# Performance work log

Hardware: AMD Instinct MI355X
Metric: run time of the kernel (lower is better)

The kernel has to match this reference:

```python
import jax, jax.numpy as jnp
import numpy as np

EPS = 1e-12  # matches torch F.normalize default eps
WEIGHT = jnp.array([1.0, 1.0, 1.0], dtype=jnp.float32)  # per-channel loss weights


def _l2norm(x, axis):
    # torch F.normalize: x / max(||x||_2, eps)
    n = jnp.sqrt(jnp.sum(x * x, axis=axis, keepdims=True))
    return x / jnp.maximum(n, EPS)


def setup_inputs() -> dict:
    key = jax.random.key(0)
    k1, k2 = jax.random.split(key)
    shape = (16, 3, 512, 512)  # [B, C, H, W]
    return {
        "x": jax.random.normal(k1, shape, dtype=jnp.float32),
        "ref": jax.random.normal(k2, shape, dtype=jnp.float32),
    }


def reference(x, ref):
    # trace(rownorm(A) @ rownorm(B)^T) == sum(rownorm(A) * rownorm(B));
    # trace(colnorm(A)^T @ colnorm(B)) == sum(colnorm(A) * colnorm(B)).
    B, C, H, W = x.shape
    # per (batch, channel) traces, vectorized over all dims
    a = jnp.sum(_l2norm(x, -1) * _l2norm(ref, -1), axis=(-2, -1)) / H  # [B, C]
    b = jnp.sum(_l2norm(x, -2) * _l2norm(ref, -2), axis=(-2, -1)) / W  # [B, C]
    a = -jnp.sum(a * WEIGHT) / B
    b = -jnp.sum(b * WEIGHT) / B
    return a + b
```

## Files before the change

kernel.cpp:

```cpp
#include <hip/hip_runtime.h>

#define B_N 16
#define C_N 3
#define H_N 512
#define W_N 512
#define PLANES (B_N * C_N)
#define ROWS_PER_BLOCK 32
#define CHUNKS (H_N / ROWS_PER_BLOCK)
#define NBLK (PLANES * CHUNKS)
#define STATS3 (W_N * 3)
#define SCALE (-1.0f / 8192.0f)
#define EPS_F 1e-12f

__global__ __launch_bounds__(256) void spl_main_kernel(
    const float* __restrict__ x, const float* __restrict__ r,
    float* __restrict__ colpart, float* __restrict__ rowpart) {
    const int p     = blockIdx.x / CHUNKS;
    const int chunk = blockIdx.x % CHUNKS;
    const int wave  = threadIdx.x >> 6;
    const int lane  = threadIdx.x & 63;

    const float* xp = x + (size_t)p * (H_N * W_N);
    const float* rp = r + (size_t)p * (H_N * W_N);

    float cxx[8] = {0, 0, 0, 0, 0, 0, 0, 0};
    float crr[8] = {0, 0, 0, 0, 0, 0, 0, 0};
    float cxr[8] = {0, 0, 0, 0, 0, 0, 0, 0};
    float rowacc = 0.0f;

    const int r0 = chunk * ROWS_PER_BLOCK;
    for (int j = 0; j < ROWS_PER_BLOCK / 4; ++j) {
        const int row = r0 + wave + 4 * j;
        const float4* xr4 = (const float4*)(xp + (size_t)row * W_N);
        const float4* rr4 = (const float4*)(rp + (size_t)row * W_N);
        const float4 xa = xr4[lane];
        const float4 xb = xr4[lane + 64];
        const float4 ra = rr4[lane];
        const float4 rb = rr4[lane + 64];

        cxx[0] += xa.x * xa.x; cxx[1] += xa.y * xa.y; cxx[2] += xa.z * xa.z; cxx[3] += xa.w * xa.w;
        cxx[4] += xb.x * xb.x; cxx[5] += xb.y * xb.y; cxx[6] += xb.z * xb.z; cxx[7] += xb.w * xb.w;
        crr[0] += ra.x * ra.x; crr[1] += ra.y * ra.y; crr[2] += ra.z * ra.z; crr[3] += ra.w * ra.w;
        crr[4] += rb.x * rb.x; crr[5] += rb.y * rb.y; crr[6] += rb.z * rb.z; crr[7] += rb.w * rb.w;
        cxr[0] += xa.x * ra.x; cxr[1] += xa.y * ra.y; cxr[2] += xa.z * ra.z; cxr[3] += xa.w * ra.w;
        cxr[4] += xb.x * rb.x; cxr[5] += xb.y * rb.y; cxr[6] += xb.z * rb.z; cxr[7] += xb.w * rb.w;

        float sxx = cxx[0] + cxx[1] + cxx[2] + cxx[3] + cxx[4] + cxx[5] + cxx[6] + cxx[7];
        float srr = crr[0] + crr[1] + crr[2] + crr[3] + crr[4] + crr[5] + crr[6] + crr[7];
        float sxr = cxr[0] + cxr[1] + cxr[2] + cxr[3] + cxr[4] + cxr[5] + cxr[6] + cxr[7];
        sxx = xa.x * xa.x + xa.y * xa.y + xa.z * xa.z + xa.w * xa.w
            + xb.x * xb.x + xb.y * xb.y + xb.z * xb.z + xb.w * xb.w;
        srr = ra.x * ra.x + ra.y * ra.y + ra.z * ra.z + ra.w * ra.w
            + rb.x * rb.x + rb.y * rb.y + rb.z * rb.z + rb.w * rb.w;
        sxr = xa.x * ra.x + xa.y * ra.y + xa.z * ra.z + xa.w * ra.w
            + xb.x * rb.x + xb.y * rb.y + xb.z * rb.z + xb.w * rb.w;
        #pragma unroll
        for (int m = 32; m > 0; m >>= 1) {
            sxx += __shfl_down(sxx, m, 64);
            srr += __shfl_down(srr, m, 64);
            sxr += __shfl_down(sxr, m, 64);
        }
        if (lane == 0) {
            const float nx = fmaxf(sqrtf(sxx), EPS_F);
            const float nr = fmaxf(sqrtf(srr), EPS_F);
            rowacc += sxr / (nx * nr);
        }
    }

    __shared__ float smem[4][STATS3];
    #pragma unroll
    for (int k = 0; k < 4; ++k) {
        const int c0 = 4 * lane + k;
        const int c1 = c0 + 256;
        smem[wave][c0 * 3 + 0] = cxx[k];
        smem[wave][c0 * 3 + 1] = crr[k];
        smem[wave][c0 * 3 + 2] = cxr[k];
        smem[wave][c1 * 3 + 0] = cxx[4 + k];
        smem[wave][c1 * 3 + 1] = crr[4 + k];
        smem[wave][c1 * 3 + 2] = cxr[4 + k];
    }
    __shared__ float rowsums[4];
    if (lane == 0) rowsums[wave] = rowacc;
    __syncthreads();

    float* cp = colpart + (size_t)blockIdx.x * STATS3;
    #pragma unroll
    for (int k = 0; k < 6; ++k) {
        const int e = threadIdx.x + 256 * k;
        cp[e] = smem[0][e] + smem[1][e] + smem[2][e] + smem[3][e];
    }
    if (threadIdx.x == 0)
        rowpart[blockIdx.x] = rowsums[0] + rowsums[1] + rowsums[2] + rowsums[3];
}

__global__ __launch_bounds__(256) void spl_reduce_kernel(
    const float* __restrict__ colpart, const float* __restrict__ rowpart,
    float* __restrict__ planesum) {
    const int p = blockIdx.x;
    float acc[6] = {0, 0, 0, 0, 0, 0};
    const float* base = colpart + (size_t)p * CHUNKS * STATS3;
    for (int c = 0; c < CHUNKS; ++c) {
        const float* bc = base + c * STATS3;
        #pragma unroll
        for (int k = 0; k < 6; ++k) acc[k] += bc[threadIdx.x + 256 * k];
    }
    __shared__ float sums[STATS3];
    #pragma unroll
    for (int k = 0; k < 6; ++k) sums[threadIdx.x + 256 * k] = acc[k];
    __syncthreads();

    float term = 0.0f;
    #pragma unroll
    for (int k = 0; k < 2; ++k) {
        const int col = threadIdx.x + 256 * k;
        const float sxx = sums[col * 3 + 0];
        const float srr = sums[col * 3 + 1];
        const float sxr = sums[col * 3 + 2];
        term += sxr / (fmaxf(sqrtf(sxx), EPS_F) * fmaxf(sqrtf(srr), EPS_F));
    }
    if (threadIdx.x < CHUNKS) term += rowpart[p * CHUNKS + threadIdx.x];

    #pragma unroll
    for (int m = 32; m > 0; m >>= 1) term += __shfl_down(term, m, 64);
    __shared__ float ws[4];
    if ((threadIdx.x & 63) == 0) ws[threadIdx.x >> 6] = term;
    __syncthreads();
    if (threadIdx.x == 0) planesum[p] = ws[0] + ws[1] + ws[2] + ws[3];
}

__global__ void spl_final_kernel(const float* __restrict__ planesum,
                                 float* __restrict__ out) {
    float v = (threadIdx.x < PLANES) ? planesum[threadIdx.x] : 0.0f;
    #pragma unroll
    for (int m = 32; m > 0; m >>= 1) v += __shfl_down(v, m, 64);
    if (threadIdx.x == 0) out[0] = SCALE * v;
}

extern "C" void kernel_launch(void* const* d_in, const int* in_sizes, int n_in,
                              void* d_out, int out_size, void* d_ws, size_t ws_size,
                              hipStream_t stream) {
    const float* x   = (const float*)d_in[0];
    const float* ref = (const float*)d_in[1];
    float* out = (float*)d_out;

    float* colpart  = (float*)d_ws;
    float* rowpart  = colpart + (size_t)NBLK * STATS3;
    float* planesum = rowpart + NBLK;

    spl_main_kernel<<<NBLK, 256, 0, stream>>>(x, ref, colpart, rowpart);
    spl_reduce_kernel<<<PLANES, 256, 0, stream>>>(colpart, rowpart, planesum);
    spl_final_kernel<<<1, 64, 0, stream>>>(planesum, out);
}
```

Baseline: 120.9 us.

## Batch row reductions after loop and fuse final reduction via last-block counter

Row statistics are now stored per row, and the cross-lane shuffle reductions run once after the fully unrolled row loop, instead of serially inside each iteration. That lets the loads for all rows be issued together rather than waiting on shuffle chains. The separate final kernel is removed: the reduce kernel uses an atomic counter, reset by the main kernel, so the last block to finish sums the plane totals. This saves one kernel launch but adds atomics and raises register pressure from the unrolled loop.

Measured after the change: 137.8 us. +13.9%, slower.

```diff
diff --git a/kernel.cpp b/kernel.cpp
--- a/kernel.cpp
+++ b/kernel.cpp
@@ -14,7 +14,11 @@
 
 __global__ __launch_bounds__(256) void spl_main_kernel(
     const float* __restrict__ x, const float* __restrict__ r,
-    float* __restrict__ colpart, float* __restrict__ rowpart) {
+    float* __restrict__ colpart, float* __restrict__ rowpart,
+    unsigned int* __restrict__ counter) {
+    if (blockIdx.x == 0 && threadIdx.x == 0)
+        __hip_atomic_store(counter, 0u, __ATOMIC_RELAXED, __HIP_MEMORY_SCOPE_AGENT);
+
     const int p     = blockIdx.x / CHUNKS;
     const int chunk = blockIdx.x % CHUNKS;
     const int wave  = threadIdx.x >> 6;
@@ -26,9 +30,10 @@
     float cxx[8] = {0, 0, 0, 0, 0, 0, 0, 0};
     float crr[8] = {0, 0, 0, 0, 0, 0, 0, 0};
     float cxr[8] = {0, 0, 0, 0, 0, 0, 0, 0};
-    float rowacc = 0.0f;
+    float rsxx[8], rsrr[8], rsxr[8];
 
     const int r0 = chunk * ROWS_PER_BLOCK;
+    #pragma unroll
     for (int j = 0; j < ROWS_PER_BLOCK / 4; ++j) {
         const int row = r0 + wave + 4 * j;
         const float4* xr4 = (const float4*)(xp + (size_t)row * W_N);
@@ -45,25 +50,30 @@
         cxr[0] += xa.x * ra.x; cxr[1] += xa.y * ra.y; cxr[2] += xa.z * ra.z; cxr[3] += xa.w * ra.w;
         cxr[4] += xb.x * rb.x; cxr[5] += xb.y * rb.y; cxr[6] += xb.z * rb.z; cxr[7] += xb.w * rb.w;
 
-        float sxx = cxx[0] + cxx[1] + cxx[2] + cxx[3] + cxx[4] + cxx[5] + cxx[6] + cxx[7];
-        float srr = crr[0] + crr[1] + crr[2] + crr[3] + crr[4] + crr[5] + crr[6] + crr[7];
-        float sxr = cxr[0] + cxr[1] + cxr[2] + cxr[3] + cxr[4] + cxr[5] + cxr[6] + cxr[7];
-        sxx = xa.x * xa.x + xa.y * xa.y + xa.z * xa.z + xa.w * xa.w
-            + xb.x * xb.x + xb.y * xb.y + xb.z * xb.z + xb.w * xb.w;
-        srr = ra.x * ra.x + ra.y * ra.y + ra.z * ra.z + ra.w * ra.w
-            + rb.x * rb.x + rb.y * rb.y + rb.z * rb.z + rb.w * rb.w;
-        sxr = xa.x * ra.x + xa.y * ra.y + xa.z * ra.z + xa.w * ra.w
-            + xb.x * rb.x + xb.y * rb.y + xb.z * rb.z + xb.w * rb.w;
+        rsxx[j] = xa.x * xa.x + xa.y * xa.y + xa.z * xa.z + xa.w * xa.w
+                + xb.x * xb.x + xb.y * xb.y + xb.z * xb.z + xb.w * xb.w;
+        rsrr[j] = ra.x * ra.x + ra.y * ra.y + ra.z * ra.z + ra.w * ra.w
+                + rb.x * rb.x + rb.y * rb.y + rb.z * rb.z + rb.w * rb.w;
+        rsxr[j] = xa.x * ra.x + xa.y * ra.y + xa.z * ra.z + xa.w * ra.w
+                + xb.x * rb.x + xb.y * rb.y + xb.z * rb.z + xb.w * rb.w;
+    }
+
+    #pragma unroll
+    for (int m = 32; m > 0; m >>= 1) {
         #pragma unroll
-        for (int m = 32; m > 0; m >>= 1) {
-            sxx += __shfl_down(sxx, m, 64);
-            srr += __shfl_down(srr, m, 64);
-            sxr += __shfl_down(sxr, m, 64);
+        for (int j = 0; j < 8; ++j) {
+            rsxx[j] += __shfl_down(rsxx[j], m, 64);
+            rsrr[j] += __shfl_down(rsrr[j], m, 64);
+            rsxr[j] += __shfl_down(rsxr[j], m, 64);
         }
-        if (lane == 0) {
-            const float nx = fmaxf(sqrtf(sxx), EPS_F);
-            const float nr = fmaxf(sqrtf(srr), EPS_F);
-            rowacc += sxr / (nx * nr);
+    }
+    float rowacc = 0.0f;
+    if (lane == 0) {
+        #pragma unroll
+        for (int j = 0; j < 8; ++j) {
+            const float nx = fmaxf(sqrtf(rsxx[j]), EPS_F);
+            const float nr = fmaxf(sqrtf(rsrr[j]), EPS_F);
+            rowacc += rsxr[j] / (nx * nr);
         }
     }
 
@@ -95,10 +105,12 @@
 
 __global__ __launch_bounds__(256) void spl_reduce_kernel(
     const float* __restrict__ colpart, const float* __restrict__ rowpart,
-    float* __restrict__ planesum) {
+    float* __restrict__ planesum, unsigned int* __restrict__ counter,
+    float* __restrict__ out) {
     const int p = blockIdx.x;
     float acc[6] = {0, 0, 0, 0, 0, 0};
     const float* base = colpart + (size_t)p * CHUNKS * STATS3;
+    #pragma unroll 4
     for (int c = 0; c < CHUNKS; ++c) {
         const float* bc = base + c * STATS3;
         #pragma unroll
@@ -122,18 +134,31 @@
 
     #pragma unroll
     for (int m = 32; m > 0; m >>= 1) term += __shfl_down(term, m, 64);
-    __shared__ float ws[4];
-    if ((threadIdx.x & 63) == 0) ws[threadIdx.x >> 6] = term;
+    __shared__ float ws4[4];
+    if ((threadIdx.x & 63) == 0) ws4[threadIdx.x >> 6] = term;
     __syncthreads();
-    if (threadIdx.x == 0) planesum[p] = ws[0] + ws[1] + ws[2] + ws[3];
-}
 
-__global__ void spl_final_kernel(const float* __restrict__ planesum,
-                                 float* __restrict__ out) {
-    float v = (threadIdx.x < PLANES) ? planesum[threadIdx.x] : 0.0f;
-    #pragma unroll
-    for (int m = 32; m > 0; m >>= 1) v += __shfl_down(v, m, 64);
-    if (threadIdx.x == 0) out[0] = SCALE * v;
+    __shared__ bool last;
+    if (threadIdx.x == 0) {
+        const float total = ws4[0] + ws4[1] + ws4[2] + ws4[3];
+        __hip_atomic_store(&planesum[p], total, __ATOMIC_RELEASE,
+                           __HIP_MEMORY_SCOPE_AGENT);
+        const unsigned int prev = __hip_atomic_fetch_add(
+            counter, 1u, __ATOMIC_ACQ_REL, __HIP_MEMORY_SCOPE_AGENT);
+        last = (prev == PLANES - 1);
+    }
+    __syncthreads();
+
+    if (last && threadIdx.x < 64) {
+        float v = (threadIdx.x < PLANES)
+                      ? __hip_atomic_load(&planesum[threadIdx.x],
+                                          __ATOMIC_ACQUIRE,
+                                          __HIP_MEMORY_SCOPE_AGENT)
+                      : 0.0f;
+        #pragma unroll
+        for (int m = 32; m > 0; m >>= 1) v += __shfl_down(v, m, 64);
+        if (threadIdx.x == 0) out[0] = SCALE * v;
+    }
 }
 
 extern "C" void kernel_launch(void* const* d_in, const int* in_sizes, int n_in,
@@ -146,8 +171,9 @@
     float* colpart  = (float*)d_ws;
     float* rowpart  = colpart + (size_t)NBLK * STATS3;
     float* planesum = rowpart + NBLK;
+    unsigned int* counter = (unsigned int*)(planesum + PLANES);
 
-    spl_main_kernel<<<NBLK, 256, 0, stream>>>(x, ref, colpart, rowpart);
-    spl_reduce_kernel<<<PLANES, 256, 0, stream>>>(colpart, rowpart, planesum);
-    spl_final_kernel<<<1, 64, 0, stream>>>(planesum, out);
+    spl_main_kernel<<<NBLK, 256, 0, stream>>>(x, ref, colpart, rowpart, counter);
+    spl_reduce_kernel<<<PLANES, 256, 0, stream>>>(colpart, rowpart, planesum,
+                                                  counter, out);
 }
```

## Halve rows per block, split reduce per plane, fuse final reduction via atomic counter

Applied to the files above, without the earlier changes.

Main kernel now handles 16 rows per block, doubling the grid to 1536 blocks, and adds an occupancy hint plus unroll 2. Dead row-sum code is removed. The reduce kernel splits each plane into two halves to double its parallelism. The third launch is replaced by a last-block-done pattern using an atomic counter that is reset in the main kernel. This removes one kernel launch and adds parallelism, but doubles the column partial traffic written by the main kernel and read by the reduce kernel.

Result: slower. 142.1 us (+17.5%).

```diff
diff --git a/kernel.cpp b/kernel.cpp
--- a/kernel.cpp
+++ b/kernel.cpp
@@ -5,16 +5,21 @@
 #define H_N 512
 #define W_N 512
 #define PLANES (B_N * C_N)
-#define ROWS_PER_BLOCK 32
+#define ROWS_PER_BLOCK 16
 #define CHUNKS (H_N / ROWS_PER_BLOCK)
 #define NBLK (PLANES * CHUNKS)
 #define STATS3 (W_N * 3)
+#define K2_BLOCKS (PLANES * 2)
 #define SCALE (-1.0f / 8192.0f)
 #define EPS_F 1e-12f
 
-__global__ __launch_bounds__(256) void spl_main_kernel(
+__global__ __launch_bounds__(256, 6) void spl_main_kernel(
     const float* __restrict__ x, const float* __restrict__ r,
-    float* __restrict__ colpart, float* __restrict__ rowpart) {
+    float* __restrict__ colpart, float* __restrict__ rowpart,
+    unsigned int* __restrict__ counter) {
+    if (blockIdx.x == 0 && threadIdx.x == 0)
+        __hip_atomic_store(counter, 0u, __ATOMIC_RELAXED, __HIP_MEMORY_SCOPE_AGENT);
+
     const int p     = blockIdx.x / CHUNKS;
     const int chunk = blockIdx.x % CHUNKS;
     const int wave  = threadIdx.x >> 6;
@@ -29,6 +34,7 @@
     float rowacc = 0.0f;
 
     const int r0 = chunk * ROWS_PER_BLOCK;
+    #pragma unroll 2
     for (int j = 0; j < ROWS_PER_BLOCK / 4; ++j) {
         const int row = r0 + wave + 4 * j;
         const float4* xr4 = (const float4*)(xp + (size_t)row * W_N);
@@ -45,15 +51,12 @@
         cxr[0] += xa.x * ra.x; cxr[1] += xa.y * ra.y; cxr[2] += xa.z * ra.z; cxr[3] += xa.w * ra.w;
         cxr[4] += xb.x * rb.x; cxr[5] += xb.y * rb.y; cxr[6] += xb.z * rb.z; cxr[7] += xb.w * rb.w;
 
-        float sxx = cxx[0] + cxx[1] + cxx[2] + cxx[3] + cxx[4] + cxx[5] + cxx[6] + cxx[7];
-        float srr = crr[0] + crr[1] + crr[2] + crr[3] + crr[4] + crr[5] + crr[6] + crr[7];
-        float sxr = cxr[0] + cxr[1] + cxr[2] + cxr[3] + cxr[4] + cxr[5] + cxr[6] + cxr[7];
-        sxx = xa.x * xa.x + xa.y * xa.y + xa.z * xa.z + xa.w * xa.w
-            + xb.x * xb.x + xb.y * xb.y + xb.z * xb.z + xb.w * xb.w;
-        srr = ra.x * ra.x + ra.y * ra.y + ra.z * ra.z + ra.w * ra.w
-            + rb.x * rb.x + rb.y * rb.y + rb.z * rb.z + rb.w * rb.w;
-        sxr = xa.x * ra.x + xa.y * ra.y + xa.z * ra.z + xa.w * ra.w
-            + xb.x * rb.x + xb.y * rb.y + xb.z * rb.z + xb.w * rb.w;
+        float sxx = xa.x * xa.x + xa.y * xa.y + xa.z * xa.z + xa.w * xa.w
+                  + xb.x * xb.x + xb.y * xb.y + xb.z * xb.z + xb.w * xb.w;
+        float srr = ra.x * ra.x + ra.y * ra.y + ra.z * ra.z + ra.w * ra.w
+                  + rb.x * rb.x + rb.y * rb.y + rb.z * rb.z + rb.w * rb.w;
+        float sxr = xa.x * ra.x + xa.y * ra.y + xa.z * ra.z + xa.w * ra.w
+                  + xb.x * rb.x + xb.y * rb.y + xb.z * rb.z + xb.w * rb.w;
         #pragma unroll
         for (int m = 32; m > 0; m >>= 1) {
             sxx += __shfl_down(sxx, m, 64);
@@ -95,45 +98,61 @@
 
 __global__ __launch_bounds__(256) void spl_reduce_kernel(
     const float* __restrict__ colpart, const float* __restrict__ rowpart,
-    float* __restrict__ planesum) {
-    const int p = blockIdx.x;
-    float acc[6] = {0, 0, 0, 0, 0, 0};
-    const float* base = colpart + (size_t)p * CHUNKS * STATS3;
+    float* __restrict__ planepart, unsigned int* __restrict__ counter,
+    float* __restrict__ out) {
+    const int p    = blockIdx.x >> 1;
+    const int half = blockIdx.x & 1;
+
+    float acc0 = 0.0f, acc1 = 0.0f, acc2 = 0.0f;
+    const float* base = colpart + (size_t)p * CHUNKS * STATS3 + half * 768;
+    #pragma unroll 4
     for (int c = 0; c < CHUNKS; ++c) {
         const float* bc = base + c * STATS3;
-        #pragma unroll
-        for (int k = 0; k < 6; ++k) acc[k] += bc[threadIdx.x + 256 * k];
+        acc0 += bc[threadIdx.x];
+        acc1 += bc[threadIdx.x + 256];
+        acc2 += bc[threadIdx.x + 512];
     }
-    __shared__ float sums[STATS3];
-    #pragma unroll
-    for (int k = 0; k < 6; ++k) sums[threadIdx.x + 256 * k] = acc[k];
+    __shared__ float sums[768];
+    sums[threadIdx.x]       = acc0;
+    sums[threadIdx.x + 256] = acc1;
+    sums[threadIdx.x + 512] = acc2;
     __syncthreads();
 
-    float term = 0.0f;
-    #pragma unroll
-    for (int k = 0; k < 2; ++k) {
-        const int col = threadIdx.x + 256 * k;
-        const float sxx = sums[col * 3 + 0];
-        const float srr = sums[col * 3 + 1];
-        const float sxr = sums[col * 3 + 2];
-        term += sxr / (fmaxf(sqrtf(sxx), EPS_F) * fmaxf(sqrtf(srr), EPS_F));
-    }
-    if (threadIdx.x < CHUNKS) term += rowpart[p * CHUNKS + threadIdx.x];
+    const float sxx = sums[3 * threadIdx.x + 0];
+    const float srr = sums[3 * threadIdx.x + 1];
+    const float sxr = sums[3 * threadIdx.x + 2];
+    float term = sxr / (fmaxf(sqrtf(sxx), EPS_F) * fmaxf(sqrtf(srr), EPS_F));
+    if (half == 0 && threadIdx.x < CHUNKS)
+        term += rowpart[p * CHUNKS + threadIdx.x];
 
     #pragma unroll
     for (int m = 32; m > 0; m >>= 1) term += __shfl_down(term, m, 64);
-    __shared__ float ws[4];
-    if ((threadIdx.x & 63) == 0) ws[threadIdx.x >> 6] = term;
+    __shared__ float ws4[4];
+    if ((threadIdx.x & 63) == 0) ws4[threadIdx.x >> 6] = term;
     __syncthreads();
-    if (threadIdx.x == 0) planesum[p] = ws[0] + ws[1] + ws[2] + ws[3];
-}
 
-__global__ void spl_final_kernel(const float* __restrict__ planesum,
-                                 float* __restrict__ out) {
-    float v = (threadIdx.x < PLANES) ? planesum[threadIdx.x] : 0.0f;
-    #pragma unroll
-    for (int m = 32; m > 0; m >>= 1) v += __shfl_down(v, m, 64);
-    if (threadIdx.x == 0) out[0] = SCALE * v;
+    __shared__ bool last;
+    if (threadIdx.x == 0) {
+        const float total = ws4[0] + ws4[1] + ws4[2] + ws4[3];
+        __hip_atomic_store(&planepart[blockIdx.x], total, __ATOMIC_RELEASE,
+                           __HIP_MEMORY_SCOPE_AGENT);
+        const unsigned int prev = __hip_atomic_fetch_add(
+            counter, 1u, __ATOMIC_ACQ_REL, __HIP_MEMORY_SCOPE_AGENT);
+        last = (prev == K2_BLOCKS - 1);
+    }
+    __syncthreads();
+
+    if (last && threadIdx.x < 64) {
+        const int t = threadIdx.x;
+        float v = __hip_atomic_load(&planepart[t], __ATOMIC_ACQUIRE,
+                                    __HIP_MEMORY_SCOPE_AGENT);
+        if (t < K2_BLOCKS - 64)
+            v += __hip_atomic_load(&planepart[t + 64], __ATOMIC_ACQUIRE,
+                                   __HIP_MEMORY_SCOPE_AGENT);
+        #pragma unroll
+        for (int m = 32; m > 0; m >>= 1) v += __shfl_down(v, m, 64);
+        if (t == 0) out[0] = SCALE * v;
+    }
 }
 
 extern "C" void kernel_launch(void* const* d_in, const int* in_sizes, int n_in,
@@ -145,9 +164,10 @@
 
     float* colpart  = (float*)d_ws;
     float* rowpart  = colpart + (size_t)NBLK * STATS3;
-    float* planesum = rowpart + NBLK;
+    float* planepart = rowpart + NBLK;
+    unsigned int* counter = (unsigned int*)(planepart + K2_BLOCKS);
 
-    spl_main_kernel<<<NBLK, 256, 0, stream>>>(x, ref, colpart, rowpart);
-    spl_reduce_kernel<<<PLANES, 256, 0, stream>>>(colpart, rowpart, planesum);
-    spl_final_kernel<<<1, 64, 0, stream>>>(planesum, out);
+    spl_main_kernel<<<NBLK, 256, 0, stream>>>(x, ref, colpart, rowpart, counter);
+    spl_reduce_kernel<<<K2_BLOCKS, 256, 0, stream>>>(colpart, rowpart, planepart,
+                                                     counter, out);
 }
```
